# Kernel tuning notes

Hardware: AMD Instinct MI355X
Metric: run time of the kernel (lower is better)

## Reference

```python
import jax, jax.numpy as jnp
import numpy as np

B, C, H, W = 8, 256, 64, 64
D = C // 8  # qk proj dim = 32
R = C // 8  # channel-SE reduction dim = 32

def setup_inputs() -> dict:
    key = jax.random.key(0)
    ks = jax.random.split(key, 10)
    s = lambda *sh: 1.0 / np.sqrt(sh[-1])
    return {
        'x':  jax.random.normal(ks[0], (B, C, H, W), jnp.float32),
        'Wq': jax.random.normal(ks[1], (D, C), jnp.float32) * s(D, C),
        'bq': jnp.zeros((D,), jnp.float32),
        'Wk': jax.random.normal(ks[2], (D, C), jnp.float32) * s(D, C),
        'bk': jnp.zeros((D,), jnp.float32),
        'Wv': jax.random.normal(ks[3], (C, C), jnp.float32) * s(C, C),
        'bv': jnp.zeros((C,), jnp.float32),
        'gamma': jnp.ones((1,), jnp.float32),
        'W1': jax.random.normal(ks[4], (R, 2 * C), jnp.float32) * s(R, 2 * C),
        'W2': jax.random.normal(ks[5], (C, R), jnp.float32) * s(C, R),
        'lamb': jnp.ones((1,), jnp.float32),
    }

def reference(x, Wq, bq, Wk, bk, Wv, bv, gamma, W1, W2, lamb):
    b, c, h, w = x.shape
    n = h * w
    xf = x.reshape(b, c, n)  # [B,C,N]
    # --- spatial self-attention (1x1 convs == matmuls over channel dim) ---
    q = jnp.einsum('dc,bcn->bnd', Wq, xf) + bq            # [B,N,D]
    k = jnp.einsum('dc,bcn->bdn', Wk, xf) + bk[:, None]   # [B,D,N]
    attn = jax.nn.softmax(jnp.einsum('bnd,bdm->bnm', q, k), axis=-1)  # [B,N,N]
    v = jnp.einsum('dc,bcn->bdn', Wv, xf) + bv[:, None]   # [B,C,N]
    # out[b,c,m] = sum_n v[b,c,n] * attn[b,m,n]  (torch: bmm(v, attn^T))
    sp = jnp.einsum('bcn,bmn->bcm', v, attn).reshape(b, c, h, w)
    sp = gamma * sp
    # --- channel SE-gate ---
    mean = jnp.mean(xf, axis=-1)                # [B,C]
    std = jnp.std(xf, axis=-1, ddof=1)          # torch.std uses unbiased (ddof=1)
    inp = jnp.concatenate([mean, std], axis=1)  # [B,2C]
    a = jax.nn.sigmoid(jax.nn.relu(inp @ W1.T) @ W2.T)  # [B,C]
    ch = lamb * a[:, :, None, None] * x
    return sp + ch + x
```

## Files before the change

kernel.cpp:

```cpp
#include <hip/hip_runtime.h>
#include <hip/hip_bf16.h>

#define Bb 8
#define Cc 256
#define Nn 4096
#define Dd 32

typedef short bf16x8 __attribute__((ext_vector_type(8)));
typedef short bf16x4 __attribute__((ext_vector_type(4)));
typedef float f32x4 __attribute__((ext_vector_type(4)));
typedef unsigned int u32;

__device__ __forceinline__ void glds16(const void* g, void* l) {
    __builtin_amdgcn_global_load_lds(
        (const __attribute__((address_space(1))) unsigned int*)g,
        (__attribute__((address_space(3))) unsigned int*)l, 16, 0, 0);
}

__device__ __forceinline__ u32 pkbf16(float a, float b) {
    return ((u32)__bfloat16_as_ushort(__float2bfloat16(b)) << 16) |
           (u32)__bfloat16_as_ushort(__float2bfloat16(a));
}

__global__ __launch_bounds__(256) void convt_kernel(
    const float* __restrict__ x, __hip_bfloat16* __restrict__ x_t,
    float* __restrict__ sum_ws, float* __restrict__ sumsq_ws)
{
    __shared__ __hip_bfloat16 tile[64][68];
    const int n0 = blockIdx.x * 64, c0 = blockIdx.y * 64, b = blockIdx.z;
    const int t = threadIdx.x;

#pragma unroll
    for (int i = 0; i < 4; i++) {
        int id = i * 256 + t;
        int row = id >> 4, col4 = id & 15;
        float4 v = *(const float4*)(x + ((size_t)(b * Cc + c0 + row)) * Nn + n0 + col4 * 4);
        bf16x4 bv;
        bv[0] = __bfloat16_as_short(__float2bfloat16(v.x));
        bv[1] = __bfloat16_as_short(__float2bfloat16(v.y));
        bv[2] = __bfloat16_as_short(__float2bfloat16(v.z));
        bv[3] = __bfloat16_as_short(__float2bfloat16(v.w));
        *(bf16x4*)((void*)&tile[row][col4 * 4]) = bv;
        float ls  = v.x + v.y + v.z + v.w;
        float ls2 = v.x * v.x + v.y * v.y + v.z * v.z + v.w * v.w;
        ls  += __shfl_xor(ls, 1, 16);  ls2 += __shfl_xor(ls2, 1, 16);
        ls  += __shfl_xor(ls, 2, 16);  ls2 += __shfl_xor(ls2, 2, 16);
        ls  += __shfl_xor(ls, 4, 16);  ls2 += __shfl_xor(ls2, 4, 16);
        ls  += __shfl_xor(ls, 8, 16);  ls2 += __shfl_xor(ls2, 8, 16);
        if ((t & 15) == 0) {
            atomicAdd(&sum_ws[b * Cc + c0 + row], ls);
            atomicAdd(&sumsq_ws[b * Cc + c0 + row], ls2);
        }
    }
    __syncthreads();
#pragma unroll
    for (int i = 0; i < 2; i++) {
        int id = i * 256 + t;
        int nl = id >> 3, cg = id & 7;
        bf16x8 o;
#pragma unroll
        for (int j = 0; j < 8; j++) o[j] = __bfloat16_as_short(tile[cg * 8 + j][nl]);
        *(bf16x8*)(x_t + ((size_t)(b * Nn + n0 + nl)) * Cc + c0 + cg * 8) = o;
    }
}

__global__ __launch_bounds__(256) void wconv_kernel(
    const float* __restrict__ Wq, const float* __restrict__ Wk, const float* __restrict__ Wv,
    __hip_bfloat16* __restrict__ w_bf)
{
    const int ct = blockIdx.x;
    const int t = threadIdx.x;
#pragma unroll
    for (int i = 0; i < 8; i++) {
        int g = i * 256 + t;
        int row = g >> 5, c8 = g & 31;
        int c0 = c8 * 8;
        int grow = ct * 64 + row;
        const float* src;
        if (grow < 32)       src = Wq + (size_t)grow * Cc + c0;
        else if (grow < 64)  src = Wk + (size_t)(grow - 32) * Cc + c0;
        else                 src = Wv + (size_t)(grow - 64) * Cc + c0;
        float4 v0 = *(const float4*)src;
        float4 v1 = *(const float4*)(src + 4);
        bf16x8 o;
        o[0] = __bfloat16_as_short(__float2bfloat16(v0.x));
        o[1] = __bfloat16_as_short(__float2bfloat16(v0.y));
        o[2] = __bfloat16_as_short(__float2bfloat16(v0.z));
        o[3] = __bfloat16_as_short(__float2bfloat16(v0.w));
        o[4] = __bfloat16_as_short(__float2bfloat16(v1.x));
        o[5] = __bfloat16_as_short(__float2bfloat16(v1.y));
        o[6] = __bfloat16_as_short(__float2bfloat16(v1.z));
        o[7] = __bfloat16_as_short(__float2bfloat16(v1.w));
        int kchunk = c0 >> 5, qd = (c0 & 31) >> 3, cg = row >> 4, rl = row & 15;
        *(bf16x8*)(w_bf + ((size_t)ct * 32 + kchunk * 4 + cg) * 512 + (qd * 16 + rl) * 8) = o;
    }
}

__global__ __launch_bounds__(256, 2) void proj_kernel(
    const __hip_bfloat16* __restrict__ x_t, const __hip_bfloat16* __restrict__ w_bf,
    const float* __restrict__ bq, const float* __restrict__ bk, const float* __restrict__ bv,
    __hip_bfloat16* __restrict__ q_ws, __hip_bfloat16* __restrict__ k_ws,
    __hip_bfloat16* __restrict__ v_ws)
{
    __shared__ __hip_bfloat16 ldsX[32 * 512];
    __shared__ __hip_bfloat16 ldsW[32 * 512];

    const int n0 = blockIdx.x * 64;
    const int ct = blockIdx.y;
    const int b  = blockIdx.z;
    const int t = threadIdx.x;
    const int w = t >> 6, lane = t & 63, quad = lane >> 4, l15 = lane & 15;

#pragma unroll
    for (int j = 0; j < 8; j++) {
        int idx = w * 8 + j;
        int kchunk = idx >> 2, ngrp = idx & 3;
        glds16(x_t + ((size_t)(b * Nn + n0 + ngrp * 16 + l15)) * Cc + kchunk * 32 + quad * 8,
               ldsX + idx * 512);
        glds16(w_bf + ((size_t)ct * 32 + idx) * 512 + lane * 8, ldsW + idx * 512);
    }
    __syncthreads();

    f32x4 acc[4];
#pragma unroll
    for (int cg = 0; cg < 4; cg++) {
        int gcol = ct * 64 + cg * 16 + l15;
        float bias = (gcol < 32) ? bq[gcol] : (gcol < 64 ? bk[gcol - 32] : bv[gcol - 64]);
        acc[cg] = (f32x4){bias, bias, bias, bias};
    }

#pragma unroll
    for (int kchunk = 0; kchunk < 8; kchunk++) {
        bf16x8 a = *(const bf16x8*)(ldsX + ((kchunk * 4 + w) * 64 + lane) * 8);
#pragma unroll
        for (int cg = 0; cg < 4; cg++) {
            bf16x8 bw = *(const bf16x8*)(ldsW + ((kchunk * 4 + cg) * 64 + lane) * 8);
            acc[cg] = __builtin_amdgcn_mfma_f32_16x16x32_bf16(a, bw, acc[cg], 0, 0, 0);
        }
    }

#pragma unroll
    for (int cg = 0; cg < 4; cg++) {
        int gcol = ct * 64 + cg * 16 + l15;
        int nb = n0 + w * 16 + quad * 4;
        if (gcol < 64) {
            __hip_bfloat16* dst = (gcol < 32) ? q_ws : k_ws;
            int d = gcol & 31;
#pragma unroll
            for (int r = 0; r < 4; r++)
                dst[((size_t)(b * Nn + nb + r)) * Dd + d] = __float2bfloat16(acc[cg][r]);
        } else {
            int c = gcol - 64;
            bf16x4 o;
#pragma unroll
            for (int r = 0; r < 4; r++) o[r] = __bfloat16_as_short(__float2bfloat16(acc[cg][r]));
            *(bf16x4*)(v_ws + ((size_t)(b * Cc + c)) * Nn + nb) = o;
        }
    }
}

__global__ __launch_bounds__(256) void gate_kernel(
    const float* __restrict__ sum_ws, const float* __restrict__ sumsq_ws,
    const float* __restrict__ W1, const float* __restrict__ W2,
    const float* __restrict__ lamb, float* __restrict__ coef)
{
    int b = blockIdx.x;
    __shared__ float inp[2 * Cc];
    __shared__ float h[32];
    int t = threadIdx.x;
    float s  = sum_ws[b * Cc + t];
    float s2 = sumsq_ws[b * Cc + t];
    float m   = s / Nn;
    float var = (s2 - (float)Nn * m * m) / (float)(Nn - 1);
    inp[t]      = m;
    inp[Cc + t] = sqrtf(fmaxf(var, 0.f));
    __syncthreads();
    if (t < 32) {
        float a = 0.f;
        for (int i = 0; i < 2 * Cc; i++) a += W1[t * (2 * Cc) + i] * inp[i];
        h[t] = fmaxf(a, 0.f);
    }
    __syncthreads();
    float g = 0.f;
#pragma unroll
    for (int r = 0; r < 32; r++) g += W2[t * 32 + r] * h[r];
    float a = 1.f / (1.f + __expf(-g));
    coef[b * Cc + t] = 1.f + lamb[0] * a;
}

__global__ __launch_bounds__(512, 2) void attn_kernel(
    const __hip_bfloat16* __restrict__ q_ws, const __hip_bfloat16* __restrict__ k_ws,
    const __hip_bfloat16* __restrict__ v_ws, const float* __restrict__ coef,
    const float* __restrict__ x, const float* __restrict__ gamma_p,
    float* __restrict__ out)
{
    extern __shared__ __hip_bfloat16 smem[];
    __hip_bfloat16* vbuf0 = smem;
    __hip_bfloat16* vbuf1 = smem + 16384;
    __hip_bfloat16* kbuf0 = smem + 32768;
    __hip_bfloat16* kbuf1 = smem + 36864;

    const int b  = blockIdx.x & 7;
    const int m0 = (blockIdx.x >> 3) * 128;
    const int t = threadIdx.x;
    const int w = t >> 6, lane = t & 63, quad = lane >> 4, l15 = lane & 15;
    const int chalf = w & 1, mf0 = (w >> 1) * 2;

    const bf16x8 aq0 = *(const bf16x8*)(q_ws + ((size_t)(b * Nn + m0 + (mf0 + 0) * 16 + l15)) * Dd + quad * 8);
    const bf16x8 aq1 = *(const bf16x8*)(q_ws + ((size_t)(b * Nn + m0 + (mf0 + 1) * 16 + l15)) * Dd + quad * 8);

    const __hip_bfloat16* vsrc[4];
#pragma unroll
    for (int j = 0; j < 4; j++) {
        int idx = w * 4 + j;
        int ch = idx >> 4, tc = idx & 15;
        vsrc[j] = v_ws + ((size_t)(b * Cc + tc * 16 + l15)) * Nn + ch * 32 + quad * 8;
    }
    const int sl15 = (l15 & 3) | ((l15 & 4) << 1) | ((l15 & 8) >> 1);
    const __hip_bfloat16* ksrc = k_ws + ((size_t)(b * Nn + w * 16 + sl15)) * Dd + quad * 8;

#pragma unroll
    for (int j = 0; j < 4; j++) glds16(vsrc[j], vbuf0 + (w * 4 + j) * 512);
    glds16(ksrc, kbuf0 + w * 512);
    __syncthreads();

    f32x4 acc[2][8];
#pragma unroll
    for (int i = 0; i < 2; i++)
#pragma unroll
        for (int j = 0; j < 8; j++) acc[i][j] = (f32x4){0.f, 0.f, 0.f, 0.f};
    float lsum0 = 0.f, lsum1 = 0.f;

    for (int it = 0; it < Nn / 64; it++) {
        if (it + 1 < Nn / 64) {
            __hip_bfloat16* vn = ((it + 1) & 1) ? vbuf1 : vbuf0;
#pragma unroll
            for (int j = 0; j < 4; j++)
                glds16(vsrc[j] + (size_t)(it + 1) * 64, vn + (w * 4 + j) * 512);
        }
        if ((it & 1) == 0 && it + 2 < Nn / 64) {
            int sl = (it >> 1) + 1;
            glds16(ksrc + (size_t)(sl * 128) * Dd, ((sl & 1) ? kbuf1 : kbuf0) + w * 512);
        }

        const __hip_bfloat16* kb = (((it >> 1) & 1) ? kbuf1 : kbuf0) + (it & 1) * 2048;
        u32 pk0[4][2], pk1[4][2];
#pragma unroll
        for (int tt = 0; tt < 4; tt++) {
            bf16x8 ak = *(const bf16x8*)(kb + (tt * 64 + lane) * 8);
            f32x4 s0 = __builtin_amdgcn_mfma_f32_16x16x32_bf16(ak, aq0, (f32x4){0.f,0.f,0.f,0.f}, 0, 0, 0);
            f32x4 s1 = __builtin_amdgcn_mfma_f32_16x16x32_bf16(ak, aq1, (f32x4){0.f,0.f,0.f,0.f}, 0, 0, 0);
            float a0 = __expf(s0[0]), a1 = __expf(s0[1]), a2 = __expf(s0[2]), a3 = __expf(s0[3]);
            lsum0 += (a0 + a1) + (a2 + a3);
            pk0[tt][0] = pkbf16(a0, a1);
            pk0[tt][1] = pkbf16(a2, a3);
            float b0 = __expf(s1[0]), b1 = __expf(s1[1]), b2 = __expf(s1[2]), b3 = __expf(s1[3]);
            lsum1 += (b0 + b1) + (b2 + b3);
            pk1[tt][0] = pkbf16(b0, b1);
            pk1[tt][1] = pkbf16(b2, b3);
        }

        const __hip_bfloat16* vb = (it & 1) ? vbuf1 : vbuf0;
#pragma unroll
        for (int nc = 0; nc < 2; nc++) {
            auto g0 = __builtin_amdgcn_permlane32_swap(pk0[2 * nc][0], pk0[2 * nc + 1][0], false, false);
            auto g1 = __builtin_amdgcn_permlane32_swap(pk0[2 * nc][1], pk0[2 * nc + 1][1], false, false);
            auto h0 = __builtin_amdgcn_permlane32_swap(pk1[2 * nc][0], pk1[2 * nc + 1][0], false, false);
            auto h1 = __builtin_amdgcn_permlane32_swap(pk1[2 * nc][1], pk1[2 * nc + 1][1], false, false);
            union { u32 uw[4]; bf16x8 v; } bp0, bp1;
            bp0.uw[0] = g0[0]; bp0.uw[1] = g1[0]; bp0.uw[2] = g0[1]; bp0.uw[3] = g1[1];
            bp1.uw[0] = h0[0]; bp1.uw[1] = h1[0]; bp1.uw[2] = h0[1]; bp1.uw[3] = h1[1];
#pragma unroll
            for (int cf = 0; cf < 8; cf++) {
                bf16x8 av = *(const bf16x8*)(vb + (((nc * 16) + chalf * 8 + cf) * 64 + lane) * 8);
                acc[0][cf] = __builtin_amdgcn_mfma_f32_16x16x32_bf16(av, bp0.v, acc[0][cf], 0, 0, 0);
                acc[1][cf] = __builtin_amdgcn_mfma_f32_16x16x32_bf16(av, bp1.v, acc[1][cf], 0, 0, 0);
            }
        }
        __syncthreads();
    }

    lsum0 += __shfl_xor(lsum0, 16); lsum0 += __shfl_xor(lsum0, 32);
    lsum1 += __shfl_xor(lsum1, 16); lsum1 += __shfl_xor(lsum1, 32);
    const float g = gamma_p[0];
    const float inv0 = g / lsum0, inv1 = g / lsum1;

#pragma unroll
    for (int cf = 0; cf < 8; cf++) {
#pragma unroll
        for (int r = 0; r < 4; r++) {
            int c = chalf * 128 + cf * 16 + quad * 4 + r;
            float cfv = coef[b * Cc + c];
            size_t base = ((size_t)(b * Cc + c)) * Nn + m0 + mf0 * 16 + l15;
            out[base]      = acc[0][cf][r] * inv0 + cfv * x[base];
            out[base + 16] = acc[1][cf][r] * inv1 + cfv * x[base + 16];
        }
    }
}

extern "C" void kernel_launch(void* const* d_in, const int* in_sizes, int n_in,
                              void* d_out, int out_size, void* d_ws, size_t ws_size,
                              hipStream_t stream) {
    const float* x     = (const float*)d_in[0];
    const float* Wq    = (const float*)d_in[1];
    const float* bq    = (const float*)d_in[2];
    const float* Wk    = (const float*)d_in[3];
    const float* bk    = (const float*)d_in[4];
    const float* Wv    = (const float*)d_in[5];
    const float* bv    = (const float*)d_in[6];
    const float* gamma = (const float*)d_in[7];
    const float* W1    = (const float*)d_in[8];
    const float* W2    = (const float*)d_in[9];
    const float* lamb  = (const float*)d_in[10];
    float* out = (float*)d_out;

    char* ws = (char*)d_ws;
    __hip_bfloat16* q_ws = (__hip_bfloat16*)ws;
    __hip_bfloat16* k_ws = (__hip_bfloat16*)(ws + (2u  << 20));
    __hip_bfloat16* v_ws = (__hip_bfloat16*)(ws + (4u  << 20));
    __hip_bfloat16* x_t  = (__hip_bfloat16*)(ws + (20u << 20));
    float* sum_ws   = (float*)(ws + (36u << 20));
    float* sumsq_ws = sum_ws + Bb * Cc;
    float* coef     = sumsq_ws + Bb * Cc;
    __hip_bfloat16* w_bf = (__hip_bfloat16*)(ws + (37u << 20));

    (void)hipFuncSetAttribute((const void*)attn_kernel,
                              hipFuncAttributeMaxDynamicSharedMemorySize, 81920);

    hipMemsetAsync(sum_ws, 0, 2 * Bb * Cc * sizeof(float), stream);
    wconv_kernel<<<5, 256, 0, stream>>>(Wq, Wk, Wv, w_bf);
    convt_kernel<<<dim3(Nn / 64, Cc / 64, Bb), 256, 0, stream>>>(x, x_t, sum_ws, sumsq_ws);
    proj_kernel<<<dim3(Nn / 64, 5, Bb), 256, 0, stream>>>(x_t, w_bf, bq, bk, bv, q_ws, k_ws, v_ws);
    gate_kernel<<<Bb, 256, 0, stream>>>(sum_ws, sumsq_ws, W1, W2, lamb, coef);
    attn_kernel<<<256, 512, 81920, stream>>>(q_ws, k_ws, v_ws, coef, x, gamma, out);
}
```

Measured before the change: 260.3 us.

## Assign each warp one query tile across all channels to avoid duplicate softmax

Reassigns attention work so each warp owns one 16-row query tile and all 256 output channels instead of two query tiles and half the channels. This removes the duplicated QK MFMAs and exp/pack computations that paired warps previously both performed. In exchange, each warp now loads every V fragment from LDS for a single MFMA instead of reusing it across two query tiles, doubling LDS read traffic for V.

```diff
diff --git a/kernel.cpp b/kernel.cpp
--- a/kernel.cpp
+++ b/kernel.cpp
@@ -204,10 +204,8 @@
     const int m0 = (blockIdx.x >> 3) * 128;
     const int t = threadIdx.x;
     const int w = t >> 6, lane = t & 63, quad = lane >> 4, l15 = lane & 15;
-    const int chalf = w & 1, mf0 = (w >> 1) * 2;
-
-    const bf16x8 aq0 = *(const bf16x8*)(q_ws + ((size_t)(b * Nn + m0 + (mf0 + 0) * 16 + l15)) * Dd + quad * 8);
-    const bf16x8 aq1 = *(const bf16x8*)(q_ws + ((size_t)(b * Nn + m0 + (mf0 + 1) * 16 + l15)) * Dd + quad * 8);
+
+    const bf16x8 aq = *(const bf16x8*)(q_ws + ((size_t)(b * Nn + m0 + w * 16 + l15)) * Dd + quad * 8);
 
     const __hip_bfloat16* vsrc[4];
 #pragma unroll
@@ -224,12 +222,10 @@
     glds16(ksrc, kbuf0 + w * 512);
     __syncthreads();
 
-    f32x4 acc[2][8];
-#pragma unroll
-    for (int i = 0; i < 2; i++)
-#pragma unroll
-        for (int j = 0; j < 8; j++) acc[i][j] = (f32x4){0.f, 0.f, 0.f, 0.f};
-    float lsum0 = 0.f, lsum1 = 0.f;
+    f32x4 acc[16];
+#pragma unroll
+    for (int j = 0; j < 16; j++) acc[j] = (f32x4){0.f, 0.f, 0.f, 0.f};
+    float lsum = 0.f;
 
     for (int it = 0; it < Nn / 64; it++) {
         if (it + 1 < Nn / 64) {
@@ -244,56 +240,45 @@
         }
 
         const __hip_bfloat16* kb = (((it >> 1) & 1) ? kbuf1 : kbuf0) + (it & 1) * 2048;
-        u32 pk0[4][2], pk1[4][2];
+        u32 pk[4][2];
 #pragma unroll
         for (int tt = 0; tt < 4; tt++) {
             bf16x8 ak = *(const bf16x8*)(kb + (tt * 64 + lane) * 8);
-            f32x4 s0 = __builtin_amdgcn_mfma_f32_16x16x32_bf16(ak, aq0, (f32x4){0.f,0.f,0.f,0.f}, 0, 0, 0);
-            f32x4 s1 = __builtin_amdgcn_mfma_f32_16x16x32_bf16(ak, aq1, (f32x4){0.f,0.f,0.f,0.f}, 0, 0, 0);
-            float a0 = __expf(s0[0]), a1 = __expf(s0[1]), a2 = __expf(s0[2]), a3 = __expf(s0[3]);
-            lsum0 += (a0 + a1) + (a2 + a3);
-            pk0[tt][0] = pkbf16(a0, a1);
-            pk0[tt][1] = pkbf16(a2, a3);
-            float b0 = __expf(s1[0]), b1 = __expf(s1[1]), b2 = __expf(s1[2]), b3 = __expf(s1[3]);
-            lsum1 += (b0 + b1) + (b2 + b3);
-            pk1[tt][0] = pkbf16(b0, b1);
-            pk1[tt][1] = pkbf16(b2, b3);
+            f32x4 s = __builtin_amdgcn_mfma_f32_16x16x32_bf16(ak, aq, (f32x4){0.f,0.f,0.f,0.f}, 0, 0, 0);
+            float a0 = __expf(s[0]), a1 = __expf(s[1]), a2 = __expf(s[2]), a3 = __expf(s[3]);
+            lsum += (a0 + a1) + (a2 + a3);
+            pk[tt][0] = pkbf16(a0, a1);
+            pk[tt][1] = pkbf16(a2, a3);
         }
 
         const __hip_bfloat16* vb = (it & 1) ? vbuf1 : vbuf0;
 #pragma unroll
         for (int nc = 0; nc < 2; nc++) {
-            auto g0 = __builtin_amdgcn_permlane32_swap(pk0[2 * nc][0], pk0[2 * nc + 1][0], false, false);
-            auto g1 = __builtin_amdgcn_permlane32_swap(pk0[2 * nc][1], pk0[2 * nc + 1][1], false, false);
-            auto h0 = __builtin_amdgcn_permlane32_swap(pk1[2 * nc][0], pk1[2 * nc + 1][0], false, false);
-            auto h1 = __builtin_amdgcn_permlane32_swap(pk1[2 * nc][1], pk1[2 * nc + 1][1], false, false);
-            union { u32 uw[4]; bf16x8 v; } bp0, bp1;
-            bp0.uw[0] = g0[0]; bp0.uw[1] = g1[0]; bp0.uw[2] = g0[1]; bp0.uw[3] = g1[1];
-            bp1.uw[0] = h0[0]; bp1.uw[1] = h1[0]; bp1.uw[2] = h0[1]; bp1.uw[3] = h1[1];
-#pragma unroll
-            for (int cf = 0; cf < 8; cf++) {
-                bf16x8 av = *(const bf16x8*)(vb + (((nc * 16) + chalf * 8 + cf) * 64 + lane) * 8);
-                acc[0][cf] = __builtin_amdgcn_mfma_f32_16x16x32_bf16(av, bp0.v, acc[0][cf], 0, 0, 0);
-                acc[1][cf] = __builtin_amdgcn_mfma_f32_16x16x32_bf16(av, bp1.v, acc[1][cf], 0, 0, 0);
+            auto g0 = __builtin_amdgcn_permlane32_swap(pk[2 * nc][0], pk[2 * nc + 1][0], false, false);
+            auto g1 = __builtin_amdgcn_permlane32_swap(pk[2 * nc][1], pk[2 * nc + 1][1], false, false);
+            union { u32 uw[4]; bf16x8 v; } bp;
+            bp.uw[0] = g0[0]; bp.uw[1] = g1[0]; bp.uw[2] = g0[1]; bp.uw[3] = g1[1];
+#pragma unroll
+            for (int cf = 0; cf < 16; cf++) {
+                bf16x8 av = *(const bf16x8*)(vb + ((nc * 16 + cf) * 64 + lane) * 8);
+                acc[cf] = __builtin_amdgcn_mfma_f32_16x16x32_bf16(av, bp.v, acc[cf], 0, 0, 0);
             }
         }
         __syncthreads();
     }
 
-    lsum0 += __shfl_xor(lsum0, 16); lsum0 += __shfl_xor(lsum0, 32);
-    lsum1 += __shfl_xor(lsum1, 16); lsum1 += __shfl_xor(lsum1, 32);
+    lsum += __shfl_xor(lsum, 16); lsum += __shfl_xor(lsum, 32);
     const float g = gamma_p[0];
-    const float inv0 = g / lsum0, inv1 = g / lsum1;
-
-#pragma unroll
-    for (int cf = 0; cf < 8; cf++) {
+    const float inv = g / lsum;
+
+#pragma unroll
+    for (int cf = 0; cf < 16; cf++) {
 #pragma unroll
         for (int r = 0; r < 4; r++) {
-            int c = chalf * 128 + cf * 16 + quad * 4 + r;
+            int c = cf * 16 + quad * 4 + r;
             float cfv = coef[b * Cc + c];
-            size_t base = ((size_t)(b * Cc + c)) * Nn + m0 + mf0 * 16 + l15;
-            out[base]      = acc[0][cf][r] * inv0 + cfv * x[base];
-            out[base + 16] = acc[1][cf][r] * inv1 + cfv * x[base + 16];
+            size_t base = ((size_t)(b * Cc + c)) * Nn + m0 + w * 16 + l15;
+            out[base] = acc[cf][r] * inv + cfv * x[base];
         }
     }
 }
```

Result: slower. 271.6 us (+4.3%).
